# Kernel tuning notes

Measured on AMD Instinct MI355X. Metric: run time of the kernel, lower is better.

The kernel has to match this reference:

```python
import jax, jax.numpy as jnp
import numpy as np
import math

B, LQ, S, D = 8, 4096, 77, 1024
H, HD = 16, 64
R, ALPHA = 192, 16.0
LORA_SCALE = ALPHA / R
N_SUBJ = 32


def setup_inputs() -> dict:
    key = jax.random.key(0)
    ks = jax.random.split(key, 16)
    w = 0.02
    return {
        "hidden_states": jax.random.normal(ks[0], (B, LQ, D), jnp.float32),
        "encoder_hidden_states": jax.random.normal(ks[1], (B, S, D), jnp.float32),
        "Wq": jax.random.normal(ks[2], (D, D), jnp.float32) * w,
        "Wk": jax.random.normal(ks[3], (D, D), jnp.float32) * w,
        "Wv": jax.random.normal(ks[4], (D, D), jnp.float32) * w,
        "Wo": jax.random.normal(ks[5], (D, D), jnp.float32) * w,
        "bo": jnp.zeros((D,), jnp.float32),
        "Ak": jax.random.normal(ks[6], (R, D), jnp.float32) * w,
        "Bk": jax.random.normal(ks[7], (D, R), jnp.float32) * w,
        "Av": jax.random.normal(ks[8], (R, D), jnp.float32) * w,
        "Bv": jax.random.normal(ks[9], (D, R), jnp.float32) * w,
        "Ao": jax.random.normal(ks[10], (R, D), jnp.float32) * w,
        "Bo": jax.random.normal(ks[11], (D, R), jnp.float32) * w,
        "cross_attn_scale_factor": jnp.ones((), jnp.float32),
        "subj_b": jax.random.randint(ks[12], (N_SUBJ,), 0, B, jnp.int32),
        "subj_n": jax.random.randint(ks[13], (N_SUBJ,), 0, S, jnp.int32),
    }


def _lora(x, A, Bm):
    # peft LoRA delta: scale * (x @ A^T) @ B^T
    return LORA_SCALE * ((x @ A.T) @ Bm.T)


def reference(hidden_states, encoder_hidden_states, Wq, Wk, Wv, Wo, bo,
              Ak, Bk, Av, Bv, Ao, Bo, cross_attn_scale_factor, subj_b, subj_n):
    hs, ehs = hidden_states, encoder_hidden_states
    # q_lora_updates_query=False -> query uses the base projection only
    q = hs @ Wq.T                                  # [B, LQ, D]
    k = ehs @ Wk.T + _lora(ehs, Ak, Bk)            # [B, S, D] (to_k_lora)
    v = ehs @ Wv.T + _lora(ehs, Av, Bv)            # [B, S, D] (to_v_lora)

    q = q.reshape(B, LQ, H, HD).transpose(0, 2, 1, 3)   # [B,H,LQ,HD]
    k = k.reshape(B, S, H, HD).transpose(0, 2, 1, 3)    # [B,H,S,HD]
    v = v.reshape(B, S, H, HD).transpose(0, 2, 1, 3)

    scale = 1.0 / math.sqrt(HD)
    attn_score = jnp.einsum('bhld,bhsd->bhls', q, k) * scale  # [B,H,LQ,S]

    # normalize_cross_attn: zero-center subject-token scores over query dim,
    # then rescale by the learned cross_attn_scale_factor.
    sub = attn_score[subj_b, :, :, subj_n]                    # [K,H,LQ]
    sub = (sub - sub.mean(axis=2, keepdims=True)) * cross_attn_scale_factor
    attn_score = attn_score.at[subj_b, :, :, subj_n].set(sub)

    attn_weight = jax.nn.softmax(attn_score, axis=-1)
    out = jnp.einsum('bhls,bhsd->bhld', attn_weight, v)       # [B,H,LQ,HD]
    out = out.transpose(0, 2, 1, 3).reshape(B, LQ, D)

    # to_out_lora: base out-proj (with bias) + LoRA delta; to_out[1] dropout = id
    out = out @ Wo.T + bo + _lora(out, Ao, Bo)
    return out
```

## Files before the change

### kernel.cpp

```cpp
#include <hip/hip_runtime.h>
#include <stdint.h>

#define B_     8
#define LQ_    4096
#define S_     77
#define SP_    80
#define D_     1024
#define H_     16
#define HD_    64
#define NC_    1280
#define NSUBJ_ 32

typedef __attribute__((ext_vector_type(4))) float  f4;
typedef __attribute__((ext_vector_type(8))) short  short8;
typedef __attribute__((ext_vector_type(8))) unsigned short us8;
typedef __attribute__((ext_vector_type(4))) unsigned short us4;

__device__ __forceinline__ unsigned short f2bf(float f) {
  union { float f; unsigned u; } x; x.f = f;
  unsigned r = x.u + 0x7FFFu + ((x.u >> 16) & 1u);
  return (unsigned short)(r >> 16);
}

__device__ __forceinline__ void gload16(const void* g, void* s) {
  __builtin_amdgcn_global_load_lds((const __attribute__((address_space(1))) void*)g,
                                   (__attribute__((address_space(3))) void*)s, 16, 0, 0);
}

__global__ __launch_bounds__(256) void k_hssum(const float* __restrict__ hs,
                                               float* __restrict__ part,
                                               unsigned short* __restrict__ hsb) {
  int b = blockIdx.y;
  size_t base = ((size_t)b * LQ_ + (size_t)blockIdx.x * 64) * D_ + threadIdx.x * 4;
  f4 acc = {0.f, 0.f, 0.f, 0.f};
  for (int l = 0; l < 64; ++l) {
    f4 v = *(const f4*)(hs + base + (size_t)l * D_);
    acc += v;
    if (hsb) {
      us4 o;
#pragma unroll
      for (int j = 0; j < 4; ++j) o[j] = f2bf(v[j]);
      *(us4*)(hsb + base + (size_t)l * D_) = o;
    }
  }
  *(f4*)(part + (size_t)blockIdx.x * (B_ * D_) + b * D_ + threadIdx.x * 4) = acc;
}

__global__ __launch_bounds__(256) void k_hsred(const float* __restrict__ part,
                                               float* __restrict__ hssum) {
  int i = blockIdx.x * 256 + threadIdx.x;
  float s = 0.f;
  for (int x = 0; x < 64; ++x) s += part[(size_t)x * (B_ * D_) + i];
  hssum[i] = s;
}

__global__ __launch_bounds__(256) void k_tr4(const float* __restrict__ Wq, const float* __restrict__ Ak,
                                             const float* __restrict__ Av, const float* __restrict__ Ao,
                                             float* __restrict__ wqT, float* __restrict__ akT,
                                             float* __restrict__ avT, float* __restrict__ aoT) {
  int z = blockIdx.z;
  const float* in = z == 0 ? Wq : (z == 1 ? Ak : (z == 2 ? Av : Ao));
  float* out = z == 0 ? wqT : (z == 1 ? akT : (z == 2 ? avT : aoT));
  int R = z == 0 ? 1024 : 192;
  const int C = 1024;
  int c0 = blockIdx.x * 32, r0 = blockIdx.y * 32;
  if (r0 >= R) return;
  __shared__ float tile[32][33];
  int tx = threadIdx.x & 31, ty = threadIdx.x >> 5;
#pragma unroll
  for (int k = 0; k < 4; ++k)
    tile[ty + 8 * k][tx] = in[(size_t)(r0 + ty + 8 * k) * C + c0 + tx];
  __syncthreads();
#pragma unroll
  for (int k = 0; k < 4; ++k)
    out[(size_t)(c0 + ty + 8 * k) * R + r0 + tx] = tile[tx][ty + 8 * k];
}

template <bool OBF>
__device__ __forceinline__ void gemm64_body(
    const float* __restrict__ A, int lda, const float* __restrict__ Bt, int ldb,
    void* __restrict__ Cv, int ldc, long cbase, const float* __restrict__ Dm, int ldd,
    int M, int Mv, int N, int K, float alpha, int m0, int n0,
    short* As, short* Bs) {
  int t = threadIdx.x, lane = t & 63, wid = t >> 6;
  int wm = wid >> 1, wn = wid & 1;
  f4 acc[2][2] = {};
  int srow = t >> 2, skc = (t & 3) * 8;
  for (int k0 = 0; k0 < K; k0 += 32) {
    __syncthreads();
    f4 a0 = {0,0,0,0}, a1 = {0,0,0,0}, b0 = {0,0,0,0}, b1 = {0,0,0,0};
    if (m0 + srow < Mv) {
      const float* p = A + (size_t)(m0 + srow) * lda + k0 + skc;
      a0 = *(const f4*)p; a1 = *(const f4*)(p + 4);
    }
    if (n0 + srow < N) {
      const float* p = Bt + (size_t)(n0 + srow) * ldb + k0 + skc;
      b0 = *(const f4*)p; b1 = *(const f4*)(p + 4);
    }
    us8 ua, ub;
#pragma unroll
    for (int j = 0; j < 4; ++j) {
      ua[j] = f2bf(a0[j]); ua[4 + j] = f2bf(a1[j]);
      ub[j] = f2bf(b0[j]); ub[4 + j] = f2bf(b1[j]);
    }
    *(us8*)(As + srow * 40 + skc) = ua;
    *(us8*)(Bs + srow * 40 + skc) = ub;
    __syncthreads();
    short8 fa[2], fb[2];
#pragma unroll
    for (int i = 0; i < 2; ++i) {
      fa[i] = *(const short8*)(As + (wm * 32 + i * 16 + (lane & 15)) * 40 + (lane >> 4) * 8);
      fb[i] = *(const short8*)(Bs + (wn * 32 + i * 16 + (lane & 15)) * 40 + (lane >> 4) * 8);
    }
#pragma unroll
    for (int mi = 0; mi < 2; ++mi)
#pragma unroll
      for (int ni = 0; ni < 2; ++ni)
        acc[mi][ni] = __builtin_amdgcn_mfma_f32_16x16x32_bf16(fa[mi], fb[ni], acc[mi][ni], 0, 0, 0);
  }
#pragma unroll
  for (int mi = 0; mi < 2; ++mi)
#pragma unroll
    for (int ni = 0; ni < 2; ++ni)
#pragma unroll
      for (int j = 0; j < 4; ++j) {
        int row = m0 + wm * 32 + mi * 16 + (lane >> 4) * 4 + j;
        int col = n0 + wn * 32 + ni * 16 + (lane & 15);
        if (row < M && col < N) {
          float val = acc[mi][ni][j] * alpha;
          if (Dm) val += Dm[(size_t)row * ldd + col];
          size_t idx = (size_t)cbase + (size_t)row * ldc + col;
          if (OBF) ((unsigned short*)Cv)[idx] = f2bf(val);
          else     ((float*)Cv)[idx] = val;
        }
      }
}

template <bool OBF>
__global__ __launch_bounds__(256) void k_gemm_small(
    const float* __restrict__ A, int lda, long sA1, long sA2,
    const float* __restrict__ Bt, int ldb, long sB1, long sB2,
    void* __restrict__ Cv, int ldc, long sC1, long sC2,
    const float* __restrict__ Dm, int ldd,
    int M, int Mv, int N, int K, float alpha, int Z2) {
  int z = blockIdx.z, z1 = z / Z2, z2 = z - z1 * Z2;
  __shared__ short As[64 * 40];
  __shared__ short Bs[64 * 40];
  gemm64_body<OBF>(A + z1 * sA1 + z2 * sA2, lda, Bt + z1 * sB1 + z2 * sB2, ldb,
                   Cv, ldc, z1 * sC1 + z2 * sC2, Dm, ldd, M, Mv, N, K, alpha,
                   blockIdx.x * 64, blockIdx.y * 64, As, Bs);
}

__global__ __launch_bounds__(256) void k_weff(
    const float* __restrict__ Bk, const float* __restrict__ Bv, const float* __restrict__ Bo,
    const float* __restrict__ akT, const float* __restrict__ avT, const float* __restrict__ aoT,
    const float* __restrict__ Wk, const float* __restrict__ Wv, const float* __restrict__ Wo,
    float* __restrict__ weff, float alpha) {
  int z = blockIdx.z;
  const float* A  = z == 0 ? Bk : (z == 1 ? Bv : Bo);
  const float* Bt = z == 0 ? akT : (z == 1 ? avT : aoT);
  const float* Dm = z == 0 ? Wk : (z == 1 ? Wv : Wo);
  __shared__ short As[64 * 40];
  __shared__ short Bs[64 * 40];
  gemm64_body<false>(A, 192, Bt, 192, weff + (size_t)z * 1048576, 1024, 0, Dm, 1024,
                     1024, 1024, 1024, 192, alpha, blockIdx.x * 64, blockIdx.y * 64, As, Bs);
}

__global__ void k_mubeta(const float* __restrict__ hssum, const float* __restrict__ Wq,
                         const float* __restrict__ kv,
                         const int* __restrict__ sb, const int* __restrict__ sn,
                         const float* __restrict__ csf_p,
                         float* __restrict__ alphav, float* __restrict__ betav) {
  int h = blockIdx.x, b = blockIdx.y;
  int t = threadIdx.x;
  __shared__ float qp[64];
  {
    int hd = t >> 1, half = t & 1;
    const float* wr = Wq + (size_t)(h * 64 + hd) * D_ + half * 512;
    const float* hp = hssum + b * D_ + half * 512;
    float s = 0.f;
    for (int d = 0; d < 512; d += 4) {
      f4 w = *(const f4*)(wr + d);
      f4 x = *(const f4*)(hp + d);
      s += w[0] * x[0] + w[1] * x[1] + w[2] * x[2] + w[3] * x[3];
    }
    s += __shfl_xor(s, 1, 64);
    if (half == 0) qp[hd] = s * (1.f / 4096.f);
  }
  __syncthreads();
  int s = t;
  if (s >= SP_) return;
  const float* kp = kv + ((size_t)(b * SP_ + s)) * 2048 + h * HD_;
  float mu = 0.f;
#pragma unroll 8
  for (int hd = 0; hd < HD_; ++hd) mu += qp[hd] * kp[hd];
  mu *= 0.125f;
  bool subj = false;
  for (int i = 0; i < NSUBJ_; ++i) subj = subj || (sb[i] == b && sn[i] == s);
  float csf = *csf_p;
  int c = b * NC_ + h * SP_ + s;
  alphav[c] = subj ? csf : 1.f;
  betav[c] = (s >= S_) ? -1e30f : (subj ? -mu * csf : 0.f);
}

__global__ __launch_bounds__(512, 2) void k_score_big(
    const unsigned short* __restrict__ hsb, const unsigned short* __restrict__ Mt,
    const float* __restrict__ alphav, const float* __restrict__ betav,
    unsigned short* __restrict__ P) {
  extern __shared__ short lds[];
  int id = blockIdx.x;
  int x = id & 7, idp = id >> 3;
  int nt = idp & 3;
  int pid = (idp >> 2) * 8 + x;
  int b = pid >> 4, mt = pid & 15;
  int m0 = mt * 256, n0 = nt * 320;

  const unsigned short* Ab = hsb + (size_t)b * LQ_ * D_;
  const unsigned short* Bb = Mt + (size_t)b * NC_ * D_;
  const float* alp = alphav + b * NC_;
  const float* bet = betav + b * NC_;
  unsigned short* Pb = P + (size_t)b * LQ_ * NC_;

  int t = threadIdx.x, lane = t & 63, wid = t >> 6;
  int wm = wid >> 2, wn = wid & 3;
  int r = lane & 15, q = lane >> 4;
  f4 acc[8][5] = {};

  auto SA = [&](int bf, int k0, int p) {
    int cb = p * 512 + wid * 64;
    int cc = cb + lane;
    int row = cc >> 2, gc = (cc & 3) ^ ((row >> 1) & 3);
    gload16(Ab + (size_t)(m0 + row) * D_ + k0 + gc * 8, (char*)(lds + bf * 8192) + cb * 16);
  };
  auto SB = [&](int bf, int k0, int p) {
    int cb = p * 512 + wid * 64;
    int cc = cb + lane;
    int row = cc >> 2, gc = (cc & 3) ^ ((row >> 1) & 3);
    gload16(Bb + (size_t)(n0 + row) * D_ + k0 + gc * 8, (char*)(lds + 32768 + bf * 10240) + cb * 16);
  };
  auto SBx = [&](int bf, int k0) {
    if (wid < 4) {
      int cb = 1024 + wid * 64;
      int cc = cb + lane;
      int row = cc >> 2, gc = (cc & 3) ^ ((row >> 1) & 3);
      gload16(Bb + (size_t)(n0 + row) * D_ + k0 + gc * 8, (char*)(lds + 32768 + bf * 10240) + cb * 16);
    }
  };
  auto STAGE_P1 = [&](int h) { if (h < 32) { int bf = h & 3, k0 = h * 32; SA(bf, k0, 0); SA(bf, k0, 1); SB(bf, k0, 0); } };
  auto STAGE_P2 = [&](int h) { if (h < 32) { int bf = h & 3, k0 = h * 32; SB(bf, k0, 1); SBx(bf, k0); } };

  STAGE_P1(0); STAGE_P2(0);
  STAGE_P1(1); STAGE_P2(1);
  STAGE_P1(2); STAGE_P2(2);
  if (wid < 4) asm volatile("s_waitcnt vmcnt(10)" ::: "memory");
  else         asm volatile("s_waitcnt vmcnt(8)" ::: "memory");
  __builtin_amdgcn_s_barrier();

#pragma unroll 1
  for (int h = 0; h < 32; ++h) {
    int bf = h & 3;
    const short* Ar = lds + bf * 8192;
    const short* Br = lds + 32768 + bf * 10240;
    short8 fa[4], fb[5];

#pragma unroll
    for (int ni = 0; ni < 5; ++ni) {
      int row = wn * 80 + ni * 16 + r;
      fb[ni] = *(const short8*)(Br + row * 32 + ((q ^ ((row >> 1) & 3)) * 8));
    }
#pragma unroll
    for (int mi = 0; mi < 4; ++mi) {
      int row = wm * 128 + mi * 16 + r;
      fa[mi] = *(const short8*)(Ar + row * 32 + ((q ^ ((row >> 1) & 3)) * 8));
    }
    __builtin_amdgcn_sched_barrier(0);
    STAGE_P1(h + 3);
    __builtin_amdgcn_sched_barrier(0);
    __builtin_amdgcn_s_barrier();
    asm volatile("s_waitcnt lgkmcnt(0)");
    __builtin_amdgcn_s_setprio(1);
#pragma unroll
    for (int mi = 0; mi < 4; ++mi)
#pragma unroll
      for (int ni = 0; ni < 5; ++ni)
        acc[mi][ni] = __builtin_amdgcn_mfma_f32_16x16x32_bf16(fa[mi], fb[ni], acc[mi][ni], 0, 0, 0);
    __builtin_amdgcn_s_setprio(0);

#pragma unroll
    for (int mi = 0; mi < 4; ++mi) {
      int row = wm * 128 + (4 + mi) * 16 + r;
      fa[mi] = *(const short8*)(Ar + row * 32 + ((q ^ ((row >> 1) & 3)) * 8));
    }
    __builtin_amdgcn_sched_barrier(0);
    STAGE_P2(h + 3);
    __builtin_amdgcn_sched_barrier(0);
    __builtin_amdgcn_s_barrier();
    asm volatile("s_waitcnt lgkmcnt(0)");
    __builtin_amdgcn_s_setprio(1);
#pragma unroll
    for (int mi = 0; mi < 4; ++mi)
#pragma unroll
      for (int ni = 0; ni < 5; ++ni)
        acc[4 + mi][ni] = __builtin_amdgcn_mfma_f32_16x16x32_bf16(fa[mi], fb[ni], acc[4 + mi][ni], 0, 0, 0);
    __builtin_amdgcn_s_setprio(0);

    if (h <= 28) {
      if (wid < 4) asm volatile("s_waitcnt vmcnt(10)" ::: "memory");
      else         asm volatile("s_waitcnt vmcnt(8)" ::: "memory");
    } else if (h == 29) {
      if (wid < 4) asm volatile("s_waitcnt vmcnt(5)" ::: "memory");
      else         asm volatile("s_waitcnt vmcnt(4)" ::: "memory");
    } else if (h == 30) {
      asm volatile("s_waitcnt vmcnt(0)" ::: "memory");
    }
    if (h < 31) __builtin_amdgcn_s_barrier();
  }

  float al[5], be[5];
#pragma unroll
  for (int ni = 0; ni < 5; ++ni) {
    int cc = n0 + wn * 80 + ni * 16 + r;
    al[ni] = alp[cc]; be[ni] = bet[cc];
  }
#pragma unroll
  for (int mi = 0; mi < 8; ++mi) {
#pragma unroll
    for (int j = 0; j < 4; ++j) {
      float v[5];
      float m = -3.0e38f;
#pragma unroll
      for (int ni = 0; ni < 5; ++ni) { v[ni] = acc[mi][ni][j] * al[ni] + be[ni]; m = fmaxf(m, v[ni]); }
#pragma unroll
      for (int off = 1; off < 16; off <<= 1) m = fmaxf(m, __shfl_xor(m, off, 64));
      float ssum = 0.f;
#pragma unroll
      for (int ni = 0; ni < 5; ++ni) { v[ni] = __expf(v[ni] - m); ssum += v[ni]; }
#pragma unroll
      for (int off = 1; off < 16; off <<= 1) ssum += __shfl_xor(ssum, off, 64);
      float inv = 1.f / ssum;
      int row = m0 + wm * 128 + mi * 16 + q * 4 + j;
      size_t rb = (size_t)row * NC_ + n0 + wn * 80 + r;
#pragma unroll
      for (int ni = 0; ni < 5; ++ni)
        Pb[rb + ni * 16] = f2bf(v[ni] * inv);
    }
  }
}

__global__ __launch_bounds__(256) void k_score_f32(
    const float* __restrict__ hs, const unsigned short* __restrict__ Mt,
    const float* __restrict__ alphav, const float* __restrict__ betav,
    unsigned short* __restrict__ P) {
  int id = blockIdx.x;
  int x = id & 7, idp = id >> 3;
  int n_t = idp & 7;
  int pid = (idp >> 3) * 8 + x;
  int b = pid >> 5, m_t = pid & 31;
  int m0 = m_t * 128, n0 = n_t * 160;
  const float* Af = hs + (size_t)b * LQ_ * D_;
  const unsigned short* Bb = Mt + (size_t)b * NC_ * D_;
  const float* alp = alphav + b * NC_;
  const float* bet = betav + b * NC_;
  unsigned short* Pb = P + (size_t)b * LQ_ * NC_;
  __shared__ short As[128 * 64];
  __shared__ short Bs[160 * 64];
  int t = threadIdx.x, lane = t & 63, wid = t >> 6;
  int wm = wid >> 1, wn = wid & 1;
  int srow = lane >> 3;
  int schunk = (lane & 7) ^ srow;
  f4 acc[4][5] = {};
  for (int k0 = 0; k0 < D_; k0 += 64) {
    __syncthreads();
    for (int i = wid; i < 20; i += 4)
      gload16(Bb + (size_t)(n0 + i * 8 + srow) * D_ + k0 + schunk * 8, (char*)Bs + i * 1024);
    int arow = t >> 3, ac = t & 7;
    int awc = ac ^ (arow & 7);
#pragma unroll
    for (int p = 0; p < 4; ++p) {
      int row = p * 32 + arow;
      const float* src = Af + (size_t)(m0 + row) * D_ + k0 + ac * 8;
      f4 v0 = *(const f4*)src;
      f4 v1 = *(const f4*)(src + 4);
      us8 u;
#pragma unroll
      for (int j = 0; j < 4; ++j) { u[j] = f2bf(v0[j]); u[4 + j] = f2bf(v1[j]); }
      *(us8*)(As + row * 64 + awc * 8) = u;
    }
    __syncthreads();
#pragma unroll
    for (int kk = 0; kk < 2; ++kk) {
      int co = ((kk * 4 + (lane >> 4)) ^ (lane & 7)) * 8;
      short8 fa[4], fb[5];
#pragma unroll
      for (int mi = 0; mi < 4; ++mi)
        fa[mi] = *(const short8*)(As + (wm * 64 + mi * 16 + (lane & 15)) * 64 + co);
#pragma unroll
      for (int ni = 0; ni < 5; ++ni)
        fb[ni] = *(const short8*)(Bs + (wn * 80 + ni * 16 + (lane & 15)) * 64 + co);
#pragma unroll
      for (int mi = 0; mi < 4; ++mi)
#pragma unroll
        for (int ni = 0; ni < 5; ++ni)
          acc[mi][ni] = __builtin_amdgcn_mfma_f32_16x16x32_bf16(fa[mi], fb[ni], acc[mi][ni], 0, 0, 0);
    }
  }
  float al[5], be[5];
#pragma unroll
  for (int ni = 0; ni < 5; ++ni) {
    int cc = n0 + wn * 80 + ni * 16 + (lane & 15);
    al[ni] = alp[cc]; be[ni] = bet[cc];
  }
#pragma unroll
  for (int mi = 0; mi < 4; ++mi) {
#pragma unroll
    for (int j = 0; j < 4; ++j) {
      float v[5];
      float m = -3.0e38f;
#pragma unroll
      for (int ni = 0; ni < 5; ++ni) { v[ni] = acc[mi][ni][j] * al[ni] + be[ni]; m = fmaxf(m, v[ni]); }
#pragma unroll
      for (int off = 1; off < 16; off <<= 1) m = fmaxf(m, __shfl_xor(m, off, 64));
      float ssum = 0.f;
#pragma unroll
      for (int ni = 0; ni < 5; ++ni) { v[ni] = __expf(v[ni] - m); ssum += v[ni]; }
#pragma unroll
      for (int off = 1; off < 16; off <<= 1) ssum += __shfl_xor(ssum, off, 64);
      float inv = 1.f / ssum;
      int row = m0 + wm * 64 + mi * 16 + (lane >> 4) * 4 + j;
      size_t rb = (size_t)row * NC_ + n0 + wn * 80 + (lane & 15);
#pragma unroll
      for (int ni = 0; ni < 5; ++ni)
        Pb[rb + ni * 16] = f2bf(v[ni] * inv);
    }
  }
}

__global__ __launch_bounds__(512, 2) void k_out_big(
    const unsigned short* __restrict__ P, const unsigned short* __restrict__ Ut,
    const float* __restrict__ bo, float* __restrict__ out) {
  extern __shared__ short lds[];
  int id = blockIdx.x;
  int x = id & 7, idp = id >> 3;
  int nt = idp & 3;
  int pid = (idp >> 2) * 8 + x;
  int b = pid >> 4, mt = pid & 15;
  int m0 = mt * 256, n0 = nt * 256;

  const unsigned short* Ab = P + (size_t)b * LQ_ * NC_;
  const unsigned short* Bb = Ut + (size_t)b * D_ * NC_;
  float* ob = out + (size_t)b * LQ_ * D_;

  int t = threadIdx.x, lane = t & 63, wid = t >> 6;
  int wm = wid >> 2, wn = wid & 3;
  int r = lane & 15, q = lane >> 4;
  f4 acc[8][4] = {};
  const int T = NC_ / 32;

  auto SA = [&](int bf, int k0, int p) {
    int cb = p * 512 + wid * 64;
    int cc = cb + lane;
    int row = cc >> 2, gc = (cc & 3) ^ ((row >> 1) & 3);
    gload16(Ab + (size_t)(m0 + row) * NC_ + k0 + gc * 8, (char*)(lds + bf * 8192) + cb * 16);
  };
  auto SB = [&](int bf, int k0, int p) {
    int cb = p * 512 + wid * 64;
    int cc = cb + lane;
    int row = cc >> 2, gc = (cc & 3) ^ ((row >> 1) & 3);
    gload16(Bb + (size_t)(n0 + row) * NC_ + k0 + gc * 8, (char*)(lds + 32768 + bf * 8192) + cb * 16);
  };
  auto STAGE_P1 = [&](int h) { if (h < T) { int bf = h & 3, k0 = h * 32; SA(bf, k0, 0); SA(bf, k0, 1); } };
  auto STAGE_P2 = [&](int h) { if (h < T) { int bf = h & 3, k0 = h * 32; SB(bf, k0, 0); SB(bf, k0, 1); } };

  STAGE_P1(0); STAGE_P2(0);
  STAGE_P1(1); STAGE_P2(1);
  STAGE_P1(2); STAGE_P2(2);
  asm volatile("s_waitcnt vmcnt(8)" ::: "memory");
  __builtin_amdgcn_s_barrier();

#pragma unroll 1
  for (int h = 0; h < T; ++h) {
    int bf = h & 3;
    const short* Ar = lds + bf * 8192;
    const short* Br = lds + 32768 + bf * 8192;
    short8 fa[4], fb[4];

#pragma unroll
    for (int ni = 0; ni < 4; ++ni) {
      int row = wn * 64 + ni * 16 + r;
      fb[ni] = *(const short8*)(Br + row * 32 + ((q ^ ((row >> 1) & 3)) * 8));
    }
#pragma unroll
    for (int mi = 0; mi < 4; ++mi) {
      int row = wm * 128 + mi * 16 + r;
      fa[mi] = *(const short8*)(Ar + row * 32 + ((q ^ ((row >> 1) & 3)) * 8));
    }
    __builtin_amdgcn_sched_barrier(0);
    STAGE_P1(h + 3);
    __builtin_amdgcn_sched_barrier(0);
    __builtin_amdgcn_s_barrier();
    asm volatile("s_waitcnt lgkmcnt(0)");
    __builtin_amdgcn_s_setprio(1);
#pragma unroll
    for (int mi = 0; mi < 4; ++mi)
#pragma unroll
      for (int ni = 0; ni < 4; ++ni)
        acc[mi][ni] = __builtin_amdgcn_mfma_f32_16x16x32_bf16(fa[mi], fb[ni], acc[mi][ni], 0, 0, 0);
    __builtin_amdgcn_s_setprio(0);

#pragma unroll
    for (int mi = 0; mi < 4; ++mi) {
      int row = wm * 128 + (4 + mi) * 16 + r;
      fa[mi] = *(const short8*)(Ar + row * 32 + ((q ^ ((row >> 1) & 3)) * 8));
    }
    __builtin_amdgcn_sched_barrier(0);
    STAGE_P2(h + 3);
    __builtin_amdgcn_sched_barrier(0);
    __builtin_amdgcn_s_barrier();
    asm volatile("s_waitcnt lgkmcnt(0)");
    __builtin_amdgcn_s_setprio(1);
#pragma unroll
    for (int mi = 0; mi < 4; ++mi)
#pragma unroll
      for (int ni = 0; ni < 4; ++ni)
        acc[4 + mi][ni] = __builtin_amdgcn_mfma_f32_16x16x32_bf16(fa[mi], fb[ni], acc[4 + mi][ni], 0, 0, 0);
    __builtin_amdgcn_s_setprio(0);

    if (h <= T - 4) {
      asm volatile("s_waitcnt vmcnt(8)" ::: "memory");
    } else if (h == T - 3) {
      asm volatile("s_waitcnt vmcnt(4)" ::: "memory");
    } else if (h == T - 2) {
      asm volatile("s_waitcnt vmcnt(0)" ::: "memory");
    }
    if (h < T - 1) __builtin_amdgcn_s_barrier();
  }

#pragma unroll
  for (int ni = 0; ni < 4; ++ni) {
    int col = n0 + wn * 64 + ni * 16 + r;
    float bov = bo[col];
#pragma unroll
    for (int mi = 0; mi < 8; ++mi)
#pragma unroll
      for (int j = 0; j < 4; ++j) {
        int row = m0 + wm * 128 + mi * 16 + q * 4 + j;
        ob[(size_t)row * D_ + col] = acc[mi][ni][j] + bov;
      }
  }
}

extern "C" void kernel_launch(void* const* d_in, const int* in_sizes, int n_in,
                              void* d_out, int out_size, void* d_ws, size_t ws_size,
                              hipStream_t stream) {
  const float* hs  = (const float*)d_in[0];
  const float* ehs = (const float*)d_in[1];
  const float* Wq  = (const float*)d_in[2];
  const float* Wk  = (const float*)d_in[3];
  const float* Wv  = (const float*)d_in[4];
  const float* Wo  = (const float*)d_in[5];
  const float* bo  = (const float*)d_in[6];
  const float* Ak  = (const float*)d_in[7];
  const float* Bk  = (const float*)d_in[8];
  const float* Av  = (const float*)d_in[9];
  const float* Bv  = (const float*)d_in[10];
  const float* Ao  = (const float*)d_in[11];
  const float* Bo  = (const float*)d_in[12];
  const float* csf = (const float*)d_in[13];
  const int*   sb  = (const int*)d_in[14];
  const int*   sn  = (const int*)d_in[15];
  float* out = (float*)d_out;

  hipFuncSetAttribute(reinterpret_cast<const void*>(k_score_big),
                      hipFuncAttributeMaxDynamicSharedMemorySize, 147456);
  hipFuncSetAttribute(reinterpret_cast<const void*>(k_out_big),
                      hipFuncAttributeMaxDynamicSharedMemorySize, 131072);

  char* ws = (char*)d_ws;
  unsigned short* P  = (unsigned short*)ws;
  unsigned short* Mt = (unsigned short*)(ws + 83886080);
  unsigned short* Ut = (unsigned short*)(ws + 104857600);
  const size_t NEED_HSB = 125829120ULL + 67108864ULL + 81920ULL;
  bool useHsb = ws_size >= NEED_HSB;
  unsigned short* hsb = useHsb ? (unsigned short*)(ws + 125829120) : nullptr;
  char* tail = useHsb ? (ws + 192937984) : (ws + 125829120);
  float* alphav = (float*)tail;
  float* betav  = (float*)(tail + 40960);
  float* kvbuf = (float*)(ws + 0);
  float* weff  = (float*)(ws + 5242880);
  float* wqT   = (float*)(ws + 17825792);
  float* aT    = (float*)(ws + 22020096);
  float* part  = (float*)(ws + 24379392);
  float* hssum = (float*)(ws + 26476544);

  float* woE = weff + 2097152;
  float* akT = aT;
  float* avT = aT + 196608;
  float* aoT = aT + 393216;

  const float LS = 16.0f / 192.0f;

  k_hssum<<<dim3(64, 8), 256, 0, stream>>>(hs, part, hsb);
  k_hsred<<<32, 256, 0, stream>>>(part, hssum);

  k_tr4<<<dim3(32, 32, 4), 256, 0, stream>>>(Wq, Ak, Av, Ao, wqT, akT, avT, aoT);

  k_weff<<<dim3(16, 16, 3), 256, 0, stream>>>(Bk, Bv, Bo, akT, avT, aoT, Wk, Wv, Wo, weff, LS);

  k_gemm_small<false><<<dim3(2, 32, 8), 256, 0, stream>>>(
      ehs, 1024, 77L * 1024, 0, weff, 1024, 0, 0, kvbuf, 2048, 80L * 2048, 0, nullptr, 0,
      80, 77, 2048, 1024, 1.f, 1);

  k_gemm_small<true><<<dim3(2, 16, 128), 256, 0, stream>>>(
      kvbuf, 2048, 80L * 2048, 64L, wqT, 1024, 0, 64L,
      Mt, 1024, (long)NC_ * 1024, 80L * 1024, nullptr, 0,
      80, 80, 1024, 64, 0.125f, 16);

  k_gemm_small<true><<<dim3(16, 2, 128), 256, 0, stream>>>(
      woE, 1024, 0, 64L, kvbuf + 1024, 2048, 80L * 2048, 64L,
      Ut, NC_, 1024L * NC_, 80L, nullptr, 0,
      1024, 1024, 80, 64, 1.f, 16);

  k_mubeta<<<dim3(16, 8), 128, 0, stream>>>(hssum, Wq, kvbuf, sb, sn, csf, alphav, betav);

  if (useHsb)
    k_score_big<<<512, 512, 147456, stream>>>(hsb, Mt, alphav, betav, P);
  else
    k_score_f32<<<2048, 256, 0, stream>>>(hs, Mt, alphav, betav, P);
  k_out_big<<<512, 512, 131072, stream>>>(P, Ut, bo, out);

  (void)in_sizes; (void)n_in; (void)out_size; (void)ws_size;
}
```

Baseline: 373.4 us.

## Convert prologue weights to bf16 and replace small GEMMs with dedicated MFMA kernels

The effective weights, the transposed Wq, the encoder states and the KV buffer are now stored in bf16 instead of fp32. The generic 64x64 k_gemm_small launches are replaced by two purpose-built MFMA kernels. k_kv computes KV with a full 80-row M tile and swizzled global-to-LDS loads. k_mtut merges the Mt and Ut products into a single launch. This targets the memory traffic and launch overhead of the prologue GEMMs, and in exchange adds bf16 rounding on intermediates such as kv and the LoRA-merged weights.

```diff
diff --git a/kernel.cpp b/kernel.cpp
--- a/kernel.cpp
+++ b/kernel.cpp
@@ -20,6 +20,10 @@
   union { float f; unsigned u; } x; x.f = f;
   unsigned r = x.u + 0x7FFFu + ((x.u >> 16) & 1u);
   return (unsigned short)(r >> 16);
+}
+__device__ __forceinline__ float bf2f(unsigned short v) {
+  union { unsigned u; float f; } x; x.u = ((unsigned)v) << 16;
+  return x.f;
 }
 
 __device__ __forceinline__ void gload16(const void* g, void* s) {
@@ -54,13 +58,26 @@
   hssum[i] = s;
 }
 
+__global__ __launch_bounds__(256) void k_ehsb(const float* __restrict__ ehs,
+                                              unsigned short* __restrict__ ehsb) {
+  int s = blockIdx.x, b = blockIdx.y;
+  int i = threadIdx.x * 4;
+  us4 o = {0, 0, 0, 0};
+  if (s < S_) {
+    f4 v = *(const f4*)(ehs + ((size_t)b * S_ + s) * D_ + i);
+#pragma unroll
+    for (int j = 0; j < 4; ++j) o[j] = f2bf(v[j]);
+  }
+  *(us4*)(ehsb + ((size_t)b * SP_ + s) * D_ + i) = o;
+}
+
 __global__ __launch_bounds__(256) void k_tr4(const float* __restrict__ Wq, const float* __restrict__ Ak,
                                              const float* __restrict__ Av, const float* __restrict__ Ao,
-                                             float* __restrict__ wqT, float* __restrict__ akT,
+                                             unsigned short* __restrict__ wqTb, float* __restrict__ akT,
                                              float* __restrict__ avT, float* __restrict__ aoT) {
   int z = blockIdx.z;
   const float* in = z == 0 ? Wq : (z == 1 ? Ak : (z == 2 ? Av : Ao));
-  float* out = z == 0 ? wqT : (z == 1 ? akT : (z == 2 ? avT : aoT));
+  float* outf = z == 1 ? akT : (z == 2 ? avT : aoT);
   int R = z == 0 ? 1024 : 192;
   const int C = 1024;
   int c0 = blockIdx.x * 32, r0 = blockIdx.y * 32;
@@ -72,8 +89,12 @@
     tile[ty + 8 * k][tx] = in[(size_t)(r0 + ty + 8 * k) * C + c0 + tx];
   __syncthreads();
 #pragma unroll
-  for (int k = 0; k < 4; ++k)
-    out[(size_t)(c0 + ty + 8 * k) * R + r0 + tx] = tile[tx][ty + 8 * k];
+  for (int k = 0; k < 4; ++k) {
+    size_t idx = (size_t)(c0 + ty + 8 * k) * R + r0 + tx;
+    float v = tile[tx][ty + 8 * k];
+    if (z == 0) wqTb[idx] = f2bf(v);
+    else        outf[idx] = v;
+  }
 }
 
 template <bool OBF>
@@ -136,38 +157,176 @@
       }
 }
 
-template <bool OBF>
-__global__ __launch_bounds__(256) void k_gemm_small(
-    const float* __restrict__ A, int lda, long sA1, long sA2,
-    const float* __restrict__ Bt, int ldb, long sB1, long sB2,
-    void* __restrict__ Cv, int ldc, long sC1, long sC2,
-    const float* __restrict__ Dm, int ldd,
-    int M, int Mv, int N, int K, float alpha, int Z2) {
-  int z = blockIdx.z, z1 = z / Z2, z2 = z - z1 * Z2;
-  __shared__ short As[64 * 40];
-  __shared__ short Bs[64 * 40];
-  gemm64_body<OBF>(A + z1 * sA1 + z2 * sA2, lda, Bt + z1 * sB1 + z2 * sB2, ldb,
-                   Cv, ldc, z1 * sC1 + z2 * sC2, Dm, ldd, M, Mv, N, K, alpha,
-                   blockIdx.x * 64, blockIdx.y * 64, As, Bs);
-}
-
 __global__ __launch_bounds__(256) void k_weff(
     const float* __restrict__ Bk, const float* __restrict__ Bv, const float* __restrict__ Bo,
     const float* __restrict__ akT, const float* __restrict__ avT, const float* __restrict__ aoT,
     const float* __restrict__ Wk, const float* __restrict__ Wv, const float* __restrict__ Wo,
-    float* __restrict__ weff, float alpha) {
+    unsigned short* __restrict__ wEb, float alpha) {
   int z = blockIdx.z;
   const float* A  = z == 0 ? Bk : (z == 1 ? Bv : Bo);
   const float* Bt = z == 0 ? akT : (z == 1 ? avT : aoT);
   const float* Dm = z == 0 ? Wk : (z == 1 ? Wv : Wo);
   __shared__ short As[64 * 40];
   __shared__ short Bs[64 * 40];
-  gemm64_body<false>(A, 192, Bt, 192, weff + (size_t)z * 1048576, 1024, 0, Dm, 1024,
-                     1024, 1024, 1024, 192, alpha, blockIdx.x * 64, blockIdx.y * 64, As, Bs);
+  gemm64_body<true>(A, 192, Bt, 192, wEb + (size_t)z * 1048576, 1024, 0, Dm, 1024,
+                    1024, 1024, 1024, 192, alpha, blockIdx.x * 64, blockIdx.y * 64, As, Bs);
+}
+
+__global__ __launch_bounds__(512) void k_kv(const unsigned short* __restrict__ ehsb,
+                                            const unsigned short* __restrict__ wEb,
+                                            unsigned short* __restrict__ kvb) {
+  __shared__ short As[80 * 64];
+  __shared__ short Bs[256 * 64];
+  int b = blockIdx.x >> 3, nt = blockIdx.x & 7;
+  int n0 = nt * 256;
+  const unsigned short* Ab = ehsb + (size_t)b * SP_ * D_;
+  int t = threadIdx.x, lane = t & 63, w = t >> 6;
+  int r = lane & 15, q = lane >> 4;
+  f4 acc[5][2] = {};
+
+  for (int k0 = 0; k0 < 1024; k0 += 64) {
+    __syncthreads();
+#pragma unroll
+    for (int p = 0; p < 6; ++p) {
+      int cb = p * 512 + w * 64;
+      if (cb < 2688) {
+        int cc = cb + lane;
+        if (cb < 640) {
+          int row = cc >> 3, gc = (cc & 7) ^ (row & 7);
+          gload16(Ab + (size_t)row * D_ + k0 + gc * 8, (char*)As + cb * 16);
+        } else {
+          int bc = cc - 640, row = bc >> 3, gc = (bc & 7) ^ (row & 7);
+          gload16(wEb + (size_t)(n0 + row) * D_ + k0 + gc * 8, (char*)Bs + (cb - 640) * 16);
+        }
+      }
+    }
+    __syncthreads();
+#pragma unroll
+    for (int kk = 0; kk < 2; ++kk) {
+      int co = ((kk * 4 + q) ^ (r & 7)) * 8;
+      short8 fa[5], fb[2];
+#pragma unroll
+      for (int mi = 0; mi < 5; ++mi)
+        fa[mi] = *(const short8*)(As + (mi * 16 + r) * 64 + co);
+#pragma unroll
+      for (int ni = 0; ni < 2; ++ni)
+        fb[ni] = *(const short8*)(Bs + (w * 32 + ni * 16 + r) * 64 + co);
+#pragma unroll
+      for (int mi = 0; mi < 5; ++mi)
+#pragma unroll
+        for (int ni = 0; ni < 2; ++ni)
+          acc[mi][ni] = __builtin_amdgcn_mfma_f32_16x16x32_bf16(fa[mi], fb[ni], acc[mi][ni], 0, 0, 0);
+    }
+  }
+#pragma unroll
+  for (int mi = 0; mi < 5; ++mi)
+#pragma unroll
+    for (int ni = 0; ni < 2; ++ni)
+#pragma unroll
+      for (int j = 0; j < 4; ++j) {
+        int s = mi * 16 + q * 4 + j;
+        int col = n0 + w * 32 + ni * 16 + r;
+        kvb[((size_t)b * SP_ + s) * 2048 + col] = f2bf(acc[mi][ni][j]);
+      }
+}
+
+__global__ __launch_bounds__(512) void k_mtut(const unsigned short* __restrict__ kvb,
+                                              const unsigned short* __restrict__ wqTb,
+                                              const unsigned short* __restrict__ wEb,
+                                              unsigned short* __restrict__ Mt,
+                                              unsigned short* __restrict__ Ut) {
+  __shared__ short Ss[80 * 64];
+  __shared__ short Ls[256 * 64];
+  int z = blockIdx.x;
+  bool mt = z < 128;
+  int zz = mt ? z : z - 128;
+  int b = zz >> 4, h = zz & 15;
+  const unsigned short* small_src = kvb + (size_t)b * SP_ * 2048 + (mt ? h * 64 : 1024 + h * 64);
+  const unsigned short* large_src = mt ? (wqTb + h * 64) : (wEb + (size_t)2048 * 1024 + h * 64);
+  int t = threadIdx.x, lane = t & 63, w = t >> 6;
+  int r = lane & 15, q = lane >> 4;
+
+#pragma unroll
+  for (int p = 0; p < 2; ++p) {
+    int cb = p * 512 + w * 64;
+    if (cb < 640) {
+      int cc = cb + lane, row = cc >> 3, gc = (cc & 7) ^ (row & 7);
+      gload16(small_src + (size_t)row * 2048 + gc * 8, (char*)Ss + cb * 16);
+    }
+  }
+
+  for (int mc = 0; mc < 4; ++mc) {
+    __syncthreads();
+#pragma unroll
+    for (int p = 0; p < 4; ++p) {
+      int cb = p * 512 + w * 64;
+      int cc = cb + lane, row = cc >> 3, gc = (cc & 7) ^ (row & 7);
+      gload16(large_src + (size_t)(mc * 256 + row) * 1024 + gc * 8, (char*)Ls + cb * 16);
+    }
+    __syncthreads();
+
+    if (mt) {
+      f4 acc[5][2] = {};
+#pragma unroll
+      for (int kk = 0; kk < 2; ++kk) {
+        int co = ((kk * 4 + q) ^ (r & 7)) * 8;
+        short8 fa[5], fb[2];
+#pragma unroll
+        for (int mi = 0; mi < 5; ++mi)
+          fa[mi] = *(const short8*)(Ss + (mi * 16 + r) * 64 + co);
+#pragma unroll
+        for (int ni = 0; ni < 2; ++ni)
+          fb[ni] = *(const short8*)(Ls + (w * 32 + ni * 16 + r) * 64 + co);
+#pragma unroll
+        for (int mi = 0; mi < 5; ++mi)
+#pragma unroll
+          for (int ni = 0; ni < 2; ++ni)
+            acc[mi][ni] = __builtin_amdgcn_mfma_f32_16x16x32_bf16(fa[mi], fb[ni], acc[mi][ni], 0, 0, 0);
+      }
+#pragma unroll
+      for (int mi = 0; mi < 5; ++mi)
+#pragma unroll
+        for (int ni = 0; ni < 2; ++ni)
+#pragma unroll
+          for (int j = 0; j < 4; ++j) {
+            int s = mi * 16 + q * 4 + j;
+            int e = mc * 256 + w * 32 + ni * 16 + r;
+            Mt[((size_t)b * NC_ + h * SP_ + s) * 1024 + e] = f2bf(acc[mi][ni][j] * 0.125f);
+          }
+    } else {
+      f4 acc[2][5] = {};
+#pragma unroll
+      for (int kk = 0; kk < 2; ++kk) {
+        int co = ((kk * 4 + q) ^ (r & 7)) * 8;
+        short8 fa[2], fb[5];
+#pragma unroll
+        for (int mi = 0; mi < 2; ++mi)
+          fa[mi] = *(const short8*)(Ls + (w * 32 + mi * 16 + r) * 64 + co);
+#pragma unroll
+        for (int ni = 0; ni < 5; ++ni)
+          fb[ni] = *(const short8*)(Ss + (ni * 16 + r) * 64 + co);
+#pragma unroll
+        for (int mi = 0; mi < 2; ++mi)
+#pragma unroll
+          for (int ni = 0; ni < 5; ++ni)
+            acc[mi][ni] = __builtin_amdgcn_mfma_f32_16x16x32_bf16(fa[mi], fb[ni], acc[mi][ni], 0, 0, 0);
+      }
+#pragma unroll
+      for (int mi = 0; mi < 2; ++mi)
+#pragma unroll
+        for (int ni = 0; ni < 5; ++ni)
+#pragma unroll
+          for (int j = 0; j < 4; ++j) {
+            int e = mc * 256 + w * 32 + mi * 16 + q * 4 + j;
+            int col = h * SP_ + ni * 16 + r;
+            Ut[((size_t)b * D_ + e) * NC_ + col] = f2bf(acc[mi][ni][j]);
+          }
+    }
+  }
 }
 
 __global__ void k_mubeta(const float* __restrict__ hssum, const float* __restrict__ Wq,
-                         const float* __restrict__ kv,
+                         const unsigned short* __restrict__ kvb,
                          const int* __restrict__ sb, const int* __restrict__ sn,
                          const float* __restrict__ csf_p,
                          float* __restrict__ alphav, float* __restrict__ betav) {
@@ -190,10 +349,14 @@
   __syncthreads();
   int s = t;
   if (s >= SP_) return;
-  const float* kp = kv + ((size_t)(b * SP_ + s)) * 2048 + h * HD_;
+  const unsigned short* kp = kvb + ((size_t)(b * SP_ + s)) * 2048 + h * HD_;
   float mu = 0.f;
-#pragma unroll 8
-  for (int hd = 0; hd < HD_; ++hd) mu += qp[hd] * kp[hd];
+#pragma unroll
+  for (int hd = 0; hd < HD_; hd += 4) {
+    us4 kv = *(const us4*)(kp + hd);
+#pragma unroll
+    for (int j = 0; j < 4; ++j) mu += qp[hd + j] * bf2f(kv[j]);
+  }
   mu *= 0.125f;
   bool subj = false;
   for (int i = 0; i < NSUBJ_; ++i) subj = subj || (sb[i] == b && sn[i] == s);
@@ -585,14 +748,14 @@
   char* tail = useHsb ? (ws + 192937984) : (ws + 125829120);
   float* alphav = (float*)tail;
   float* betav  = (float*)(tail + 40960);
-  float* kvbuf = (float*)(ws + 0);
-  float* weff  = (float*)(ws + 5242880);
-  float* wqT   = (float*)(ws + 17825792);
-  float* aT    = (float*)(ws + 22020096);
-  float* part  = (float*)(ws + 24379392);
-  float* hssum = (float*)(ws + 26476544);
-
-  float* woE = weff + 2097152;
+  unsigned short* kvb   = (unsigned short*)(ws + 0);
+  unsigned short* wEb   = (unsigned short*)(ws + 2621440);
+  unsigned short* wqTb  = (unsigned short*)(ws + 8912896);
+  float*          aT    = (float*)(ws + 11010048);
+  unsigned short* ehsb  = (unsigned short*)(ws + 13369344);
+  float*          part  = (float*)(ws + 14680064);
+  float*          hssum = (float*)(ws + 16777216);
+
   float* akT = aT;
   float* avT = aT + 196608;
   float* aoT = aT + 393216;
@@ -602,25 +765,16 @@
   k_hssum<<<dim3(64, 8), 256, 0, stream>>>(hs, part, hsb);
   k_hsred<<<32, 256, 0, stream>>>(part, hssum);
 
-  k_tr4<<<dim3(32, 32, 4), 256, 0, stream>>>(Wq, Ak, Av, Ao, wqT, akT, avT, aoT);
-
-  k_weff<<<dim3(16, 16, 3), 256, 0, stream>>>(Bk, Bv, Bo, akT, avT, aoT, Wk, Wv, Wo, weff, LS);
-
-  k_gemm_small<false><<<dim3(2, 32, 8), 256, 0, stream>>>(
-      ehs, 1024, 77L * 1024, 0, weff, 1024, 0, 0, kvbuf, 2048, 80L * 2048, 0, nullptr, 0,
-      80, 77, 2048, 1024, 1.f, 1);
-
-  k_gemm_small<true><<<dim3(2, 16, 128), 256, 0, stream>>>(
-      kvbuf, 2048, 80L * 2048, 64L, wqT, 1024, 0, 64L,
-      Mt, 1024, (long)NC_ * 1024, 80L * 1024, nullptr, 0,
-      80, 80, 1024, 64, 0.125f, 16);
-
-  k_gemm_small<true><<<dim3(16, 2, 128), 256, 0, stream>>>(
-      woE, 1024, 0, 64L, kvbuf + 1024, 2048, 80L * 2048, 64L,
-      Ut, NC_, 1024L * NC_, 80L, nullptr, 0,
-      1024, 1024, 80, 64, 1.f, 16);
-
-  k_mubeta<<<dim3(16, 8), 128, 0, stream>>>(hssum, Wq, kvbuf, sb, sn, csf, alphav, betav);
+  k_tr4<<<dim3(32, 32, 4), 256, 0, stream>>>(Wq, Ak, Av, Ao, wqTb, akT, avT, aoT);
+  k_ehsb<<<dim3(SP_, B_), 256, 0, stream>>>(ehs, ehsb);
+
+  k_weff<<<dim3(16, 16, 3), 256, 0, stream>>>(Bk, Bv, Bo, akT, avT, aoT, Wk, Wv, Wo, wEb, LS);
+
+  k_kv<<<64, 512, 0, stream>>>(ehsb, wEb, kvb);
+
+  k_mtut<<<256, 512, 0, stream>>>(kvb, wqTb, wEb, Mt, Ut);
+
+  k_mubeta<<<dim3(16, 8), 128, 0, stream>>>(hssum, Wq, kvb, sb, sn, csf, alphav, betav);
 
   if (useHsb)
     k_score_big<<<512, 512, 147456, stream>>>(hsb, Mt, alphav, betav, P);
```

New measurement: 344.2 us. 7.8% less time.
